# Kernel optimization log

Measured on AMD Instinct MI355X. Metric: run time of the kernel, lower is better.

The kernel has to match this reference:

```python
import jax, jax.numpy as jnp
import numpy as np

K_SIZE = 5


def extract_patches(x, k):
    """tf.image.extract_patches(SAME, stride 1) -> [B, H, W, k*k, C].

    Kernel offsets are ordered row-major (ki, kj), matching TF's depth
    ordering (ki, kj, c) after the reshape in the original module.
    """
    pad = k // 2
    B, H, W, C = x.shape
    xp = jnp.pad(x, ((0, 0), (pad, pad), (pad, pad), (0, 0)))
    slices = [xp[:, i:i + H, j:j + W, :] for i in range(k) for j in range(k)]
    return jnp.stack(slices, axis=3)  # [B, H, W, k*k, C]


def setup_inputs() -> dict:
    key = jax.random.key(0)
    k1, k2, k3, k4, k5 = jax.random.split(key, 5)
    B, H, C, BIN = 4, 128, 128, 64
    return {
        "main": jax.random.normal(k1, (B, H, H, C), dtype=jnp.float32),
        "ref": jax.random.normal(k2, (B, H, H, C), dtype=jnp.float32),
        "ref_value": jax.random.normal(k3, (B, H, H, BIN), dtype=jnp.float32),
        "W_main": jax.random.normal(k4, (C, C), dtype=jnp.float32) * (2.0 / C) ** 0.5,
        "W_ref": jax.random.normal(k5, (C, C), dtype=jnp.float32) * (2.0 / C) ** 0.5,
    }


def reference(main, ref, ref_value, W_main, W_ref):
    k = K_SIZE
    # 1x1 convolutions (no bias) == per-pixel matmul
    conv_main = jnp.einsum('bhwc,cd->bhwd', main, W_main)
    conv_ref = jnp.einsum('bhwc,cd->bhwd', ref, W_ref)
    # local k x k neighborhood of keys: [B, H, W, k*k, C]
    ref_stacked = extract_patches(conv_ref, k)
    # dot-product attention over the local window
    attn = jnp.einsum('bhwc,bhwkc->bhwk', conv_main, ref_stacked)
    attn = jax.nn.softmax(attn, axis=-1)
    # local k x k neighborhood of values: [B, H, W, k*k, bin]
    ref_value_stacked = extract_patches(ref_value, k)
    # weighted sum of values
    return jnp.einsum('bhwk,bhwki->bhwi', attn, ref_value_stacked)
```

## Files before the change

### kernel.cpp

```cpp
#include <hip/hip_runtime.h>

#define BATCH 4
#define HH 128
#define WW 128
#define CC 128
#define BIN 64
#define NPIX (BATCH * HH * WW)

typedef short bf16x8 __attribute__((ext_vector_type(8)));
typedef float f32x4 __attribute__((ext_vector_type(4)));

__device__ __forceinline__ unsigned bf_hi(float f) {
    unsigned u = __float_as_uint(f);
    return (u + 0x7fffu + ((u >> 16) & 1u)) >> 16;
}
__device__ __forceinline__ uint2 split_aa(float f) {
    unsigned hb = bf_hi(f);
    float lo = f - __uint_as_float(hb << 16);
    unsigned lb = bf_hi(lo);
    return make_uint2(hb | (hb << 16), lb | (lb << 16));
}
__device__ __forceinline__ unsigned split_b(float f) {
    unsigned hb = bf_hi(f);
    float lo = f - __uint_as_float(hb << 16);
    unsigned lb = bf_hi(lo);
    return hb | (lb << 16);
}

#define AROW 72

__global__ __launch_bounds__(256, 3)
void conv_mfma_kernel(const float* __restrict__ Xm, const float* __restrict__ Xr,
                      const float* __restrict__ Wm, const float* __restrict__ Wr,
                      float* __restrict__ Ym, float* __restrict__ Yr) {
    const float* __restrict__ X = blockIdx.y ? Xr : Xm;
    const float* __restrict__ W = blockIdx.y ? Wr : Wm;
    float* __restrict__ Y       = blockIdx.y ? Yr : Ym;

    __shared__ unsigned short AT[128 * AROW];
    __shared__ unsigned short BT[128 * AROW];

    const int t  = threadIdx.x;
    const int wv = t >> 6;
    const int l  = t & 63;
    const int wm = (wv >> 1) * 64;
    const int wn = (wv & 1) * 64;
    const int lr = l & 15;
    const int lq = l >> 4;
    const int p_base = blockIdx.x * 128;

    const int px = t >> 1, ahalf = t & 1;
    const int d  = t & 127, bq = t >> 7;

    f32x4 acc[4][4] = {};

    for (int kc = 0; kc < CC; kc += 16) {
        __syncthreads();
        {
            const float* xp = X + (size_t)(p_base + px) * CC + kc + ahalf * 8;
            unsigned short* arow = &AT[px * AROW + ahalf * 32];
#pragma unroll
            for (int i = 0; i < 2; ++i) {
                float4 v = *(const float4*)(xp + 4 * i);
                uint2 a0 = split_aa(v.x), a1 = split_aa(v.y),
                      a2 = split_aa(v.z), a3 = split_aa(v.w);
                *(uint4*)(arow + 16 * i)     = make_uint4(a0.x, a0.y, a1.x, a1.y);
                *(uint4*)(arow + 16 * i + 8) = make_uint4(a2.x, a2.y, a3.x, a3.y);
            }
        }
        {
#pragma unroll
            for (int j = 0; j < 2; ++j) {
                const int cg = bq * 2 + j;
                const float* wp = W + (size_t)(kc + cg * 4) * CC + d;
                unsigned b0 = split_b(wp[0]);
                unsigned b1 = split_b(wp[CC]);
                unsigned b2 = split_b(wp[2 * CC]);
                unsigned b3 = split_b(wp[3 * CC]);
                unsigned short* brow = &BT[d * AROW + cg * 16];
                *(uint4*)(brow)     = make_uint4(b0, b0, b1, b1);
                *(uint4*)(brow + 8) = make_uint4(b2, b2, b3, b3);
            }
        }
        __syncthreads();
#pragma unroll
        for (int ks = 0; ks < 2; ++ks) {
            bf16x8 af[4], bfr[4];
#pragma unroll
            for (int mi = 0; mi < 4; ++mi)
                af[mi] = *(const bf16x8*)&AT[(wm + mi * 16 + lr) * AROW + ks * 32 + lq * 8];
#pragma unroll
            for (int ni = 0; ni < 4; ++ni)
                bfr[ni] = *(const bf16x8*)&BT[(wn + ni * 16 + lr) * AROW + ks * 32 + lq * 8];
#pragma unroll
            for (int mi = 0; mi < 4; ++mi)
#pragma unroll
                for (int ni = 0; ni < 4; ++ni)
                    acc[mi][ni] = __builtin_amdgcn_mfma_f32_16x16x32_bf16(
                        af[mi], bfr[ni], acc[mi][ni], 0, 0, 0);
        }
    }

#pragma unroll
    for (int mi = 0; mi < 4; ++mi)
#pragma unroll
        for (int ni = 0; ni < 4; ++ni)
#pragma unroll
            for (int reg = 0; reg < 4; ++reg) {
                const int row = p_base + wm + mi * 16 + lq * 4 + reg;
                Y[(size_t)row * CC + wn + ni * 16 + lr] = acc[mi][ni][reg];
            }
}

#define TH 8
#define TW 16
#define HALO_W 20
#define HPX 240
#define NSLOT 1920

__global__ __launch_bounds__(128, 1)
void attn_tile_kernel(const float* __restrict__ qm, const float* __restrict__ kr,
                      const float* __restrict__ vv, float* __restrict__ out) {
    __shared__ float4 KS[2][NSLOT];

    const int t   = threadIdx.x;
    const int wid = t >> 6;
    const int ln  = t & 63;

    const int bi = blockIdx.x >> 7;
    const int ty = (blockIdx.x >> 3) & 15;
    const int tx = blockIdx.x & 7;
    const int h0 = ty * TH, w0 = tx * TW;
    const int r = t >> 4, c = t & 15;
    const int h = h0 + r, w = w0 + c;
    const int gbase = bi * HH * WW;
    const int pix = gbase + h * WW + w;

    unsigned vm = 0;
#pragma unroll
    for (int dy = 0; dy < 5; ++dy)
#pragma unroll
        for (int dx = 0; dx < 5; ++dx) {
            const int hh = h + dy - 2, ww = w + dx - 2;
            if ((unsigned)hh < (unsigned)HH && (unsigned)ww < (unsigned)WW)
                vm |= 1u << (dy * 5 + dx);
        }

    auto stage = [&](int p, int buf) {
        const float* src = (p < 4) ? kr : vv;
        const int ld = (p < 4) ? CC : BIN;
        const int ch = (p < 4) ? p * 32 : (p - 4) * 32;
        for (int i = wid; i < NSLOT / 64; i += 2) {
            const int s   = i * 64 + ln;
            const int g   = s / HPX;
            const int px  = s - g * HPX;
            const int py  = px / HALO_W;
            const int pxx = px - py * HALO_W;
            int hh = h0 + py - 2;  hh = hh < 0 ? 0 : (hh > HH - 1 ? HH - 1 : hh);
            int ww = w0 + pxx - 2; ww = ww < 0 ? 0 : (ww > WW - 1 ? WW - 1 : ww);
            const float* gp = src + (size_t)(gbase + hh * WW + ww) * ld + ch + g * 4;
            __builtin_amdgcn_global_load_lds(
                (const __attribute__((address_space(1))) void*)gp,
                (__attribute__((address_space(3))) void*)&KS[buf][i * 64],
                16, 0, 0);
        }
    };

    float lg[25];
#pragma unroll
    for (int i = 0; i < 25; ++i) lg[i] = 0.0f;

    stage(0, 0);
    __syncthreads();

    for (int p = 0; p < 6; ++p) {
        if (p < 5) stage(p + 1, (p + 1) & 1);
        const float4* B = KS[p & 1];
        if (p < 4) {
            float4 q[8];
            const float4* qp = (const float4*)(qm + (size_t)pix * CC + p * 32);
#pragma unroll
            for (int g = 0; g < 8; ++g) q[g] = qp[g];
#pragma unroll
            for (int dy = 0; dy < 5; ++dy)
#pragma unroll
                for (int dx = 0; dx < 5; ++dx) {
                    const int hp = (r + dy) * HALO_W + (c + dx);
                    float part = 0.0f;
#pragma unroll
                    for (int g = 0; g < 8; ++g) {
                        float4 kv = B[g * HPX + hp];
                        part += q[g].x * kv.x + q[g].y * kv.y +
                                q[g].z * kv.z + q[g].w * kv.w;
                    }
                    lg[dy * 5 + dx] += part;
                }
        } else {
            if (p == 4) {
#pragma unroll
                for (int kk = 0; kk < 25; ++kk)
                    if (!((vm >> kk) & 1)) lg[kk] = 0.0f;
                float mx = lg[0];
#pragma unroll
                for (int kk = 1; kk < 25; ++kk) mx = fmaxf(mx, lg[kk]);
                float sum = 0.0f;
#pragma unroll
                for (int kk = 0; kk < 25; ++kk) {
                    lg[kk] = __expf(lg[kk] - mx);
                    sum += lg[kk];
                }
                const float inv = 1.0f / sum;
#pragma unroll
                for (int kk = 0; kk < 25; ++kk)
                    lg[kk] = ((vm >> kk) & 1) ? lg[kk] * inv : 0.0f;
            }
            float4 va[8];
#pragma unroll
            for (int g = 0; g < 8; ++g) va[g] = make_float4(0.f, 0.f, 0.f, 0.f);
#pragma unroll
            for (int dy = 0; dy < 5; ++dy)
#pragma unroll
                for (int dx = 0; dx < 5; ++dx) {
                    const float wgt = lg[dy * 5 + dx];
                    const int hp = (r + dy) * HALO_W + (c + dx);
#pragma unroll
                    for (int g = 0; g < 8; ++g) {
                        float4 v = B[g * HPX + hp];
                        va[g].x += wgt * v.x; va[g].y += wgt * v.y;
                        va[g].z += wgt * v.z; va[g].w += wgt * v.w;
                    }
                }
            float4* op = (float4*)(out + (size_t)pix * BIN + (p - 4) * 32);
#pragma unroll
            for (int g = 0; g < 8; ++g) op[g] = va[g];
        }
        __syncthreads();
    }
}

extern "C" void kernel_launch(void* const* d_in, const int* in_sizes, int n_in,
                              void* d_out, int out_size, void* d_ws, size_t ws_size,
                              hipStream_t stream) {
    const float* main_in   = (const float*)d_in[0];
    const float* ref_in    = (const float*)d_in[1];
    const float* ref_value = (const float*)d_in[2];
    const float* W_main    = (const float*)d_in[3];
    const float* W_ref     = (const float*)d_in[4];
    float* out = (float*)d_out;

    float* conv_main = (float*)d_ws;
    float* conv_ref  = conv_main + (size_t)NPIX * CC;

    dim3 gconv(NPIX / 128, 2);
    conv_mfma_kernel<<<gconv, 256, 0, stream>>>(main_in, ref_in, W_main, W_ref,
                                                conv_main, conv_ref);

    attn_tile_kernel<<<512, 128, 0, stream>>>(conv_main, conv_ref, ref_value, out);
}
```

Measured before the change: 192.5 us.

## Split attention channels across 4 threads per pixel and prefetch conv operands

The attention kernel now uses 512 threads per block, with four threads per pixel each handling a quarter of the channel chunk. Partial logits are combined with xor shuffles before the softmax. The halo row stride becomes 21 with 256-slot groups, which simplifies the slot index math and may reduce LDS bank conflicts. The conv kernel prefetches the next K-chunk of X and W into registers to overlap global loads with MFMA work and raises its launch-bounds occupancy hint. The risks are extra register pressure and shuffle overhead, and 64KB of LDS per block limits how many blocks can be resident.

```diff
diff --git a/kernel.cpp b/kernel.cpp
--- a/kernel.cpp
+++ b/kernel.cpp
@@ -29,7 +29,7 @@
 
 #define AROW 72
 
-__global__ __launch_bounds__(256, 3)
+__global__ __launch_bounds__(256, 4)
 void conv_mfma_kernel(const float* __restrict__ Xm, const float* __restrict__ Xr,
                       const float* __restrict__ Wm, const float* __restrict__ Wr,
                       float* __restrict__ Ym, float* __restrict__ Yr) {
@@ -54,35 +54,66 @@
 
     f32x4 acc[4][4] = {};
 
+    const float* xbase = X + (size_t)(p_base + px) * CC + ahalf * 8;
+
+    float4 xa0 = *(const float4*)(xbase);
+    float4 xa1 = *(const float4*)(xbase + 4);
+    float wb[8];
+#pragma unroll
+    for (int j = 0; j < 2; ++j) {
+        const int cg = bq * 2 + j;
+        const float* wp = W + (size_t)(cg * 4) * CC + d;
+        wb[j * 4 + 0] = wp[0];
+        wb[j * 4 + 1] = wp[CC];
+        wb[j * 4 + 2] = wp[2 * CC];
+        wb[j * 4 + 3] = wp[3 * CC];
+    }
+
     for (int kc = 0; kc < CC; kc += 16) {
         __syncthreads();
         {
-            const float* xp = X + (size_t)(p_base + px) * CC + kc + ahalf * 8;
             unsigned short* arow = &AT[px * AROW + ahalf * 32];
-#pragma unroll
-            for (int i = 0; i < 2; ++i) {
-                float4 v = *(const float4*)(xp + 4 * i);
-                uint2 a0 = split_aa(v.x), a1 = split_aa(v.y),
-                      a2 = split_aa(v.z), a3 = split_aa(v.w);
-                *(uint4*)(arow + 16 * i)     = make_uint4(a0.x, a0.y, a1.x, a1.y);
-                *(uint4*)(arow + 16 * i + 8) = make_uint4(a2.x, a2.y, a3.x, a3.y);
+            {
+                uint2 a0 = split_aa(xa0.x), a1 = split_aa(xa0.y),
+                      a2 = split_aa(xa0.z), a3 = split_aa(xa0.w);
+                *(uint4*)(arow)     = make_uint4(a0.x, a0.y, a1.x, a1.y);
+                *(uint4*)(arow + 8) = make_uint4(a2.x, a2.y, a3.x, a3.y);
+            }
+            {
+                uint2 a0 = split_aa(xa1.x), a1 = split_aa(xa1.y),
+                      a2 = split_aa(xa1.z), a3 = split_aa(xa1.w);
+                *(uint4*)(arow + 16) = make_uint4(a0.x, a0.y, a1.x, a1.y);
+                *(uint4*)(arow + 24) = make_uint4(a2.x, a2.y, a3.x, a3.y);
             }
         }
         {
 #pragma unroll
             for (int j = 0; j < 2; ++j) {
                 const int cg = bq * 2 + j;
-                const float* wp = W + (size_t)(kc + cg * 4) * CC + d;
-                unsigned b0 = split_b(wp[0]);
-                unsigned b1 = split_b(wp[CC]);
-                unsigned b2 = split_b(wp[2 * CC]);
-                unsigned b3 = split_b(wp[3 * CC]);
+                unsigned b0 = split_b(wb[j * 4 + 0]);
+                unsigned b1 = split_b(wb[j * 4 + 1]);
+                unsigned b2 = split_b(wb[j * 4 + 2]);
+                unsigned b3 = split_b(wb[j * 4 + 3]);
                 unsigned short* brow = &BT[d * AROW + cg * 16];
                 *(uint4*)(brow)     = make_uint4(b0, b0, b1, b1);
                 *(uint4*)(brow + 8) = make_uint4(b2, b2, b3, b3);
             }
         }
         __syncthreads();
+        if (kc + 16 < CC) {
+            const float* xp = xbase + kc + 16;
+            xa0 = *(const float4*)(xp);
+            xa1 = *(const float4*)(xp + 4);
+#pragma unroll
+            for (int j = 0; j < 2; ++j) {
+                const int cg = bq * 2 + j;
+                const float* wp = W + (size_t)(kc + 16 + cg * 4) * CC + d;
+                wb[j * 4 + 0] = wp[0];
+                wb[j * 4 + 1] = wp[CC];
+                wb[j * 4 + 2] = wp[2 * CC];
+                wb[j * 4 + 3] = wp[3 * CC];
+            }
+        }
 #pragma unroll
         for (int ks = 0; ks < 2; ++ks) {
             bf16x8 af[4], bfr[4];
@@ -114,27 +145,30 @@
 
 #define TH 8
 #define TW 16
-#define HALO_W 20
-#define HPX 240
-#define NSLOT 1920
-
-__global__ __launch_bounds__(128, 1)
+#define HROW 21
+#define GSLOT 256
+#define NSLOT 2048
+
+__global__ __launch_bounds__(512, 4)
 void attn_tile_kernel(const float* __restrict__ qm, const float* __restrict__ kr,
                       const float* __restrict__ vv, float* __restrict__ out) {
     __shared__ float4 KS[2][NSLOT];
 
-    const int t   = threadIdx.x;
-    const int wid = t >> 6;
-    const int ln  = t & 63;
+    const int t    = threadIdx.x;
+    const int wid  = t >> 6;
+    const int ln   = t & 63;
+    const int part = t & 3;
+    const int pxi  = t >> 2;
 
     const int bi = blockIdx.x >> 7;
     const int ty = (blockIdx.x >> 3) & 15;
     const int tx = blockIdx.x & 7;
     const int h0 = ty * TH, w0 = tx * TW;
-    const int r = t >> 4, c = t & 15;
+    const int r = pxi >> 4, c = pxi & 15;
     const int h = h0 + r, w = w0 + c;
     const int gbase = bi * HH * WW;
     const int pix = gbase + h * WW + w;
+    const int g0 = part * 2;
 
     unsigned vm = 0;
 #pragma unroll
@@ -150,12 +184,12 @@
         const float* src = (p < 4) ? kr : vv;
         const int ld = (p < 4) ? CC : BIN;
         const int ch = (p < 4) ? p * 32 : (p - 4) * 32;
-        for (int i = wid; i < NSLOT / 64; i += 2) {
+        for (int i = wid; i < NSLOT / 64; i += 8) {
             const int s   = i * 64 + ln;
-            const int g   = s / HPX;
-            const int px  = s - g * HPX;
-            const int py  = px / HALO_W;
-            const int pxx = px - py * HALO_W;
+            const int g   = s >> 8;
+            const int px  = s & 255;
+            const int py  = px / 21;
+            const int pxx = px - py * 21;
             int hh = h0 + py - 2;  hh = hh < 0 ? 0 : (hh > HH - 1 ? HH - 1 : hh);
             int ww = w0 + pxx - 2; ww = ww < 0 ? 0 : (ww > WW - 1 ? WW - 1 : ww);
             const float* gp = src + (size_t)(gbase + hh * WW + ww) * ld + ch + g * 4;
@@ -177,26 +211,29 @@
         if (p < 5) stage(p + 1, (p + 1) & 1);
         const float4* B = KS[p & 1];
         if (p < 4) {
-            float4 q[8];
-            const float4* qp = (const float4*)(qm + (size_t)pix * CC + p * 32);
-#pragma unroll
-            for (int g = 0; g < 8; ++g) q[g] = qp[g];
+            const float4* qp = (const float4*)(qm + (size_t)pix * CC + p * 32 + part * 8);
+            float4 q0 = qp[0], q1 = qp[1];
 #pragma unroll
             for (int dy = 0; dy < 5; ++dy)
 #pragma unroll
                 for (int dx = 0; dx < 5; ++dx) {
-                    const int hp = (r + dy) * HALO_W + (c + dx);
-                    float part = 0.0f;
-#pragma unroll
-                    for (int g = 0; g < 8; ++g) {
-                        float4 kv = B[g * HPX + hp];
-                        part += q[g].x * kv.x + q[g].y * kv.y +
-                                q[g].z * kv.z + q[g].w * kv.w;
-                    }
-                    lg[dy * 5 + dx] += part;
+                    const int hp = (r + dy) * HROW + (c + dx);
+                    float4 k0 = B[g0 * GSLOT + hp];
+                    float4 k1 = B[g0 * GSLOT + GSLOT + hp];
+                    lg[dy * 5 + dx] += q0.x * k0.x + q0.y * k0.y +
+                                       q0.z * k0.z + q0.w * k0.w +
+                                       q1.x * k1.x + q1.y * k1.y +
+                                       q1.z * k1.z + q1.w * k1.w;
                 }
         } else {
             if (p == 4) {
+#pragma unroll
+                for (int kk = 0; kk < 25; ++kk) {
+                    float v = lg[kk];
+                    v += __shfl_xor(v, 1);
+                    v += __shfl_xor(v, 2);
+                    lg[kk] = v;
+                }
 #pragma unroll
                 for (int kk = 0; kk < 25; ++kk)
                     if (!((vm >> kk) & 1)) lg[kk] = 0.0f;
@@ -214,25 +251,24 @@
                 for (int kk = 0; kk < 25; ++kk)
                     lg[kk] = ((vm >> kk) & 1) ? lg[kk] * inv : 0.0f;
             }
-            float4 va[8];
-#pragma unroll
-            for (int g = 0; g < 8; ++g) va[g] = make_float4(0.f, 0.f, 0.f, 0.f);
+            float4 a0 = make_float4(0.f, 0.f, 0.f, 0.f);
+            float4 a1 = make_float4(0.f, 0.f, 0.f, 0.f);
 #pragma unroll
             for (int dy = 0; dy < 5; ++dy)
 #pragma unroll
                 for (int dx = 0; dx < 5; ++dx) {
                     const float wgt = lg[dy * 5 + dx];
-                    const int hp = (r + dy) * HALO_W + (c + dx);
-#pragma unroll
-                    for (int g = 0; g < 8; ++g) {
-                        float4 v = B[g * HPX + hp];
-                        va[g].x += wgt * v.x; va[g].y += wgt * v.y;
-                        va[g].z += wgt * v.z; va[g].w += wgt * v.w;
-                    }
-                }
-            float4* op = (float4*)(out + (size_t)pix * BIN + (p - 4) * 32);
-#pragma unroll
-            for (int g = 0; g < 8; ++g) op[g] = va[g];
+                    const int hp = (r + dy) * HROW + (c + dx);
+                    float4 v0 = B[g0 * GSLOT + hp];
+                    float4 v1 = B[g0 * GSLOT + GSLOT + hp];
+                    a0.x += wgt * v0.x; a0.y += wgt * v0.y;
+                    a0.z += wgt * v0.z; a0.w += wgt * v0.w;
+                    a1.x += wgt * v1.x; a1.y += wgt * v1.y;
+                    a1.z += wgt * v1.z; a1.w += wgt * v1.w;
+                }
+            float4* op = (float4*)(out + (size_t)pix * BIN + (p - 4) * 32 + part * 8);
+            op[0] = a0;
+            op[1] = a1;
         }
         __syncthreads();
     }
@@ -255,5 +291,5 @@
     conv_mfma_kernel<<<gconv, 256, 0, stream>>>(main_in, ref_in, W_main, W_ref,
                                                 conv_main, conv_ref);
 
-    attn_tile_kernel<<<512, 128, 0, stream>>>(conv_main, conv_ref, ref_value, out);
-}
+    attn_tile_kernel<<<512, 512, 0, stream>>>(conv_main, conv_ref, ref_value, out);
+}
```

After: 189.7 us. About the same (-1.5%).
